# Kernel tuning notes

Measured on AMD Instinct MI355X. Metric: run time of the kernel, lower is better.

Reference implementation:

```python
import jax, jax.numpy as jnp
import numpy as np

N = 38332          # poi_len - 1 nodes
POI_LEN = 38333
GF = 64            # graph_features
POI_DIM = 128
C = 128            # gcn_channel
L = 4              # gcn_layers
OUT = 128          # graph_out_dim
E = N * 16         # edges (avg degree 16)
IN_DIM = POI_DIM * GF // 2 + GF // 2  # 4128


def leaky(x, s):
    return jnp.where(x >= 0, x, s * x)


def _gcn(x, W, b, src, dst):
    # PyG GCNConv: lin -> symmetric deg^{-1/2} norm over self-loop graph -> scatter-sum + bias
    h = x @ W
    deg = jax.ops.segment_sum(jnp.ones(src.shape[0], h.dtype), dst, num_segments=N)
    dinv = jnp.where(deg > 0, jax.lax.rsqrt(deg), 0.0)
    norm = dinv[src] * dinv[dst]
    return jax.ops.segment_sum(h[src] * norm[:, None], dst, num_segments=N) + b


def _gat(x, W, a_src, a_dst, b, src, dst):
    # PyG GATConv (heads=1): per-edge LeakyReLU(0.2) logits, softmax over incoming edges
    h = x @ W
    als = h @ a_src            # [N]
    ald = h @ a_dst            # [N]
    e = leaky(als[src] + ald[dst], 0.2)   # [E+N]
    m = jax.ops.segment_max(e, dst, num_segments=N)
    ex = jnp.exp(e - m[dst])
    s = jax.ops.segment_sum(ex, dst, num_segments=N)
    alpha = ex / s[dst]
    return jax.ops.segment_sum(h[src] * alpha[:, None], dst, num_segments=N) + b


def _gnorm(x, w, b, ms, eps=1e-5):
    # PyG GraphNorm over the single graph (node axis)
    mean = x.mean(axis=0)
    out = x - ms * mean
    var = (out * out).mean(axis=0)
    return w * out * jax.lax.rsqrt(var + eps) + b


def setup_inputs() -> dict:
    key = jax.random.key(0)
    ks = jax.random.split(key, 20)
    d = {}
    d["poi"] = jax.random.randint(ks[0], (N, GF // 2), 0, POI_LEN, dtype=jnp.int32)
    d["distance"] = jax.random.uniform(ks[1], (N, GF // 2), dtype=jnp.float32)
    d["edge_index"] = jax.random.randint(ks[2], (2, E), 0, N, dtype=jnp.int32)
    d["emb_table"] = jax.random.normal(ks[3], (POI_LEN, POI_DIM), dtype=jnp.float32) * 0.05
    d["W_in"] = jax.random.normal(ks[4], (IN_DIM, C), dtype=jnp.float32) * 0.02
    d["b_in"] = jnp.zeros((C,), jnp.float32)
    d["gcn_W"] = jax.random.normal(ks[5], (L, C, C), dtype=jnp.float32) * 0.05
    d["gcn_b"] = jnp.zeros((L, C), jnp.float32)
    d["norm_w"] = jnp.ones((L, C), jnp.float32)
    d["norm_b"] = jnp.zeros((L, C), jnp.float32)
    d["norm_ms"] = jnp.ones((L, C), jnp.float32)
    d["gat_W"] = jax.random.normal(ks[6], (L, C, C), dtype=jnp.float32) * 0.05
    d["gat_asrc"] = jax.random.normal(ks[7], (L, C), dtype=jnp.float32) * 0.05
    d["gat_adst"] = jax.random.normal(ks[8], (L, C), dtype=jnp.float32) * 0.05
    d["gat_b"] = jnp.zeros((L, C), jnp.float32)
    d["W_out"] = jax.random.normal(ks[9], (C, 1), dtype=jnp.float32) * 0.05
    d["b_out"] = jnp.zeros((1,), jnp.float32)
    d["fc1_W"] = jax.random.normal(ks[10], (N, 128), dtype=jnp.float32) * 0.01
    d["fc1_b"] = jnp.zeros((128,), jnp.float32)
    d["fc2_W"] = jax.random.normal(ks[11], (128, OUT), dtype=jnp.float32) * 0.05
    d["fc2_b"] = jnp.zeros((OUT,), jnp.float32)
    return d


def reference(poi, distance, edge_index, emb_table, W_in, b_in, gcn_W, gcn_b,
              norm_w, norm_b, norm_ms, gat_W, gat_asrc, gat_adst, gat_b,
              W_out, b_out, fc1_W, fc1_b, fc2_W, fc2_b):
    loops = jnp.arange(N, dtype=edge_index.dtype)
    src = jnp.concatenate([edge_index[0], loops])   # self loops (PyG default)
    dst = jnp.concatenate([edge_index[1], loops])
    # feature assembly: emb(poi) flattened || distance
    x = jnp.concatenate([emb_table[poi].reshape(N, -1), distance], axis=1)  # [N, 4128]
    x = leaky(_gcn(x, W_in, b_in, src, dst), 0.01)
    for i in range(L):  # GcnUnit: GCN->norm->lrelu->res, GAT->norm->lrelu->res (shared norm params)
        t = _gnorm(_gcn(x, gcn_W[i], gcn_b[i], src, dst), norm_w[i], norm_b[i], norm_ms[i])
        x = x + leaky(t, 0.01)
        t = _gnorm(_gat(x, gat_W[i], gat_asrc[i], gat_adst[i], gat_b[i], src, dst),
                   norm_w[i], norm_b[i], norm_ms[i])
        x = x + leaky(t, 0.01)
    x = leaky(_gcn(x, W_out, b_out, src, dst), 0.01).reshape(-1)  # [N]
    h = leaky(x @ fc1_W + fc1_b, 0.01)
    return h @ fc2_W + fc2_b  # [128]
```

## Files before the change

### kernel.cpp

```cpp
#include <hip/hip_runtime.h>


typedef _Float16 f16;
typedef f16 f16x8 __attribute__((ext_vector_type(8)));
typedef f16 f16x4 __attribute__((ext_vector_type(4)));
typedef f16 f16x2 __attribute__((ext_vector_type(2)));
typedef float f32x4 __attribute__((ext_vector_type(4)));

__device__ __forceinline__ float lrelu(float x, float s){ return x>=0.f? x : s*x; }

__global__ __launch_bounds__(256) void k_deg(const int* __restrict__ dst,
                                             int* __restrict__ deg, int E) {
  int i = blockIdx.x * 256 + threadIdx.x;
  if (i < E) atomicAdd(&deg[dst[i]], 1);
}

__global__ __launch_bounds__(1024) void k_scan1(const int* __restrict__ deg,
    int* __restrict__ row_ptr, int* __restrict__ bsum, float* __restrict__ dinv, int n) {
  int b = blockIdx.x, t = threadIdx.x, i = b * 1024 + t;
  __shared__ int sd[1024];
  int v = (i < n) ? deg[i] : 0;
  if (i < n) dinv[i] = rsqrtf((float)(v + 1));
  sd[t] = v;
  __syncthreads();
  for (int off = 1; off < 1024; off <<= 1) {
    int o = (t >= off) ? sd[t - off] : 0;
    __syncthreads();
    sd[t] += o;
    __syncthreads();
  }
  if (i < n) row_ptr[i + 1] = sd[t];
  if (t == 1023) bsum[b] = sd[1023];
  if (b == 0 && t == 0) row_ptr[0] = 0;
}

__global__ __launch_bounds__(64) void k_scan2(int* __restrict__ bsum, int nb) {
  int lane = threadIdx.x;
  int v = (lane < nb) ? bsum[lane] : 0;
  int x = v;
  for (int off = 1; off < 64; off <<= 1) {
    int o = __shfl_up(x, off, 64);
    if (lane >= off) x += o;
  }
  if (lane < nb) bsum[lane] = x - v;
}

__global__ __launch_bounds__(256) void k_scan3(int* __restrict__ row_ptr,
                                               const int* __restrict__ bsum, int n) {
  int i = blockIdx.x * 256 + threadIdx.x;
  if (i < n) row_ptr[i + 1] += bsum[i >> 10];
}

__global__ __launch_bounds__(256) void k_fill(const int* __restrict__ src,
                                              const int* __restrict__ dst,
                                              const int* __restrict__ row_ptr,
                                              const float* __restrict__ dinv,
                                              int* __restrict__ fill,
                                              int* __restrict__ csr,
                                              float* __restrict__ csrw, int E) {
  int i = blockIdx.x * 256 + threadIdx.x;
  if (i < E) {
    int d = dst[i], s = src[i];
    int pos = row_ptr[d] + atomicAdd(&fill[d], 1);
    csr[pos] = s;
    csrw[pos] = dinv[d] * dinv[s];
  }
}

__global__ __launch_bounds__(256) void k_conv_emb(const float* __restrict__ src,
                                                  f16* __restrict__ dst, int total4) {
  int i = blockIdx.x * 256 + threadIdx.x;
  if (i >= total4) return;
  float4 v = ((const float4*)src)[i];
  f16x4 o = { (f16)v.x, (f16)v.y, (f16)v.z, (f16)v.w };
  ((f16x4*)dst)[i] = o;
}

__global__ __launch_bounds__(256) void k_pack_w(const float* __restrict__ W,
    f16* __restrict__ hi, int kb_total) {
  int idx = blockIdx.x * 256 + threadIdx.x;
  int c = idx & 127, kb = idx >> 7;
  if (kb >= kb_total) return;
  f16x8 hv;
#pragma unroll
  for (int j = 0; j < 8; j++) hv[j] = (f16)W[(size_t)(kb*8 + j) * 128 + c];
  ((f16x8*)hi)[idx] = hv;
}

__global__ __launch_bounds__(256) void k_pack_w8(const float* __restrict__ gcnW,
    const float* __restrict__ gatW, f16* __restrict__ hi, f16* __restrict__ lo) {
  int mat = blockIdx.y;
  const float* W = (mat < 4) ? gcnW + (size_t)mat * 16384 : gatW + (size_t)(mat - 4) * 16384;
  int idx = blockIdx.x * 256 + threadIdx.x;
  int c = idx & 127, kb = idx >> 7;
  f16x8 hv, lv;
#pragma unroll
  for (int j = 0; j < 8; j++) {
    float v = W[(size_t)(kb*8 + j) * 128 + c];
    f16 h = (f16)v;
    hv[j] = h; lv[j] = (f16)(v - (float)h);
  }
  ((f16x8*)hi)[mat * 2048 + idx] = hv;
  ((f16x8*)lo)[mat * 2048 + idx] = lv;
}

#define APAD 152
__global__ __launch_bounds__(512) void k_mfma_embed(const int* __restrict__ poi,
    const float* __restrict__ dist, const f16* __restrict__ eh,
    const f16* __restrict__ wh, f16* __restrict__ H16, int n) {
  __shared__ __attribute__((aligned(16))) char smem[49152];
  int* poi_s = (int*)smem;
  f16* aS    = (f16*)(smem + 8192);
  f16* OT    = (f16*)smem;
  float* F   = (float*)(smem + 16384);
  int tid = threadIdx.x;
  int bn = blockIdx.x * 64;
  int half = tid >> 8;
  int t2 = tid & 255;
  int ln = t2 >> 2, qt = t2 & 3;
  int xrow = bn + ln; if (xrow > n - 1) xrow = n - 1;
  {
#pragma unroll
    for (int jj = 0; jj < 4; jj++)
      poi_s[half * 1024 + (qt * 4 + jj) * 64 + ln] =
        poi[(size_t)xrow * 32 + half * 16 + qt * 4 + jj];
  }
  int w2 = (tid >> 6) & 3, lane = tid & 63;
  int q = lane >> 4, l15 = lane & 15;
  int mtb = (w2 & 1) * 2;
  int ntb = (w2 >> 1) * 4;
  f16* aH = aS + half * 64 * APAD;
  f32x4 acc[2][4];
#pragma unroll
  for (int a = 0; a < 2; a++)
#pragma unroll
    for (int b = 0; b < 4; b++) { acc[a][b][0]=0.f; acc[a][b][1]=0.f; acc[a][b][2]=0.f; acc[a][b][3]=0.f; }
  __syncthreads();

  f16x8 A0, A1, A2, A3, B0, B1, B2, B3;
  {
    const f16* sp = eh + (size_t)poi_s[half * 1024 + 0 * 64 + ln] * 128 + qt * 32;
    A0 = *(const f16x8*)(sp);      A1 = *(const f16x8*)(sp + 8);
    A2 = *(const f16x8*)(sp + 16); A3 = *(const f16x8*)(sp + 24);
  }
  {
    const f16* sp = eh + (size_t)poi_s[half * 1024 + 1 * 64 + ln] * 128 + qt * 32;
    B0 = *(const f16x8*)(sp);      B1 = *(const f16x8*)(sp + 8);
    B2 = *(const f16x8*)(sp + 16); B3 = *(const f16x8*)(sp + 24);
  }
  f16* wp = aH + ln * APAD + qt * 32;

#pragma unroll 1
  for (int jj = 0; jj < 8; jj++) {
    int j0 = jj * 2;
    __syncthreads();
    *(f16x8*)(wp) = A0; *(f16x8*)(wp + 8) = A1;
    *(f16x8*)(wp + 16) = A2; *(f16x8*)(wp + 24) = A3;
    if (jj < 7) {
      const f16* sp = eh + (size_t)poi_s[half * 1024 + (j0 + 2) * 64 + ln] * 128 + qt * 32;
      A0 = *(const f16x8*)(sp);      A1 = *(const f16x8*)(sp + 8);
      A2 = *(const f16x8*)(sp + 16); A3 = *(const f16x8*)(sp + 24);
    }
    __syncthreads();
#pragma unroll
    for (int kcl = 0; kcl < 4; kcl++) {
      f16x8 a_h[2];
#pragma unroll
      for (int mi = 0; mi < 2; mi++)
        a_h[mi] = *(const f16x8*)(aH + ((mtb + mi) * 16 + l15) * APAD + kcl * 32 + q * 8);
      int kb = (half * 16 + j0) * 16 + kcl * 4 + q;
#pragma unroll
      for (int ni = 0; ni < 4; ni++) {
        f16x8 bh = *(const f16x8*)(wh + ((size_t)kb * 128 + (ntb + ni) * 16 + l15) * 8);
#pragma unroll
        for (int mi = 0; mi < 2; mi++)
          acc[mi][ni] = __builtin_amdgcn_mfma_f32_16x16x32_f16(a_h[mi], bh, acc[mi][ni], 0, 0, 0);
      }
    }
    __syncthreads();
    *(f16x8*)(wp) = B0; *(f16x8*)(wp + 8) = B1;
    *(f16x8*)(wp + 16) = B2; *(f16x8*)(wp + 24) = B3;
    if (jj < 7) {
      const f16* sp = eh + (size_t)poi_s[half * 1024 + (j0 + 3) * 64 + ln] * 128 + qt * 32;
      B0 = *(const f16x8*)(sp);      B1 = *(const f16x8*)(sp + 8);
      B2 = *(const f16x8*)(sp + 16); B3 = *(const f16x8*)(sp + 24);
    }
    __syncthreads();
#pragma unroll
    for (int kcl = 0; kcl < 4; kcl++) {
      f16x8 a_h[2];
#pragma unroll
      for (int mi = 0; mi < 2; mi++)
        a_h[mi] = *(const f16x8*)(aH + ((mtb + mi) * 16 + l15) * APAD + kcl * 32 + q * 8);
      int kb = (half * 16 + j0 + 1) * 16 + kcl * 4 + q;
#pragma unroll
      for (int ni = 0; ni < 4; ni++) {
        f16x8 bh = *(const f16x8*)(wh + ((size_t)kb * 128 + (ntb + ni) * 16 + l15) * 8);
#pragma unroll
        for (int mi = 0; mi < 2; mi++)
          acc[mi][ni] = __builtin_amdgcn_mfma_f32_16x16x32_f16(a_h[mi], bh, acc[mi][ni], 0, 0, 0);
      }
    }
  }
  if (half) {
    int nc0 = bn + (mtb + 0) * 16 + l15; if (nc0 > n - 1) nc0 = n - 1;
    int nc1 = bn + (mtb + 1) * 16 + l15; if (nc1 > n - 1) nc1 = n - 1;
    f16x8 ad[2];
#pragma unroll
    for (int mi = 0; mi < 2; mi++) {
      int nc = mi ? nc1 : nc0;
      const float* dp = dist + (size_t)nc * 32 + q * 8;
      float4 d0 = *(const float4*)dp, d1 = *(const float4*)(dp + 4);
      ad[mi][0]=(f16)d0.x; ad[mi][1]=(f16)d0.y; ad[mi][2]=(f16)d0.z; ad[mi][3]=(f16)d0.w;
      ad[mi][4]=(f16)d1.x; ad[mi][5]=(f16)d1.y; ad[mi][6]=(f16)d1.z; ad[mi][7]=(f16)d1.w;
    }
    int kb = 512 + q;
#pragma unroll
    for (int ni = 0; ni < 4; ni++) {
      f16x8 bh = *(const f16x8*)(wh + ((size_t)kb * 128 + (ntb + ni) * 16 + l15) * 8);
#pragma unroll
      for (int mi = 0; mi < 2; mi++)
        acc[mi][ni] = __builtin_amdgcn_mfma_f32_16x16x32_f16(ad[mi], bh, acc[mi][ni], 0, 0, 0);
    }
  }
  __syncthreads();
  if (half) {
#pragma unroll
    for (int mi = 0; mi < 2; mi++)
#pragma unroll
      for (int ni = 0; ni < 4; ni++)
#pragma unroll
        for (int r = 0; r < 4; r++)
          F[((mtb + mi) * 16 + q * 4 + r) * 128 + (ntb + ni) * 16 + l15] = acc[mi][ni][r];
  }
  __syncthreads();
  if (!half) {
#pragma unroll
    for (int mi = 0; mi < 2; mi++)
#pragma unroll
      for (int ni = 0; ni < 4; ni++)
#pragma unroll
        for (int r = 0; r < 4; r++) {
          int o = ((mtb + mi) * 16 + q * 4 + r) * 128 + (ntb + ni) * 16 + l15;
          OT[o] = (f16)(acc[mi][ni][r] + F[o]);
        }
  }
  __syncthreads();
#pragma unroll
  for (int ch = 0; ch < 2; ch++) {
    int c1024 = tid + ch * 512;
    int row = c1024 >> 4, c8 = c1024 & 15;
    if (bn + row < n)
      *(f16x8*)(H16 + (size_t)(bn + row) * 128 + c8 * 8) = *(const f16x8*)(OT + row * 128 + c8 * 8);
  }
}

#define LPAD 136
__global__ __launch_bounds__(256) void k_mfma_lin(const f16* __restrict__ XH,
    const f16* __restrict__ wh, const f16* __restrict__ wl,
    f16* __restrict__ H16, int n,
    const float* __restrict__ asrc, const float* __restrict__ adst,
    float* __restrict__ als, float* __restrict__ ald,
    const float* __restrict__ yres, const float* __restrict__ scA,
    const float* __restrict__ shA, float* __restrict__ xf) {
  __shared__ __attribute__((aligned(16))) char smem[64 * LPAD * 2];
  f16* aS = (f16*)smem;
  f16* ot = (f16*)smem;
  float* dsrc = (float*)(smem + 16384);
  float* ddst = (float*)(smem + 16896);
  int tid = threadIdx.x;
  int bn = blockIdx.x * 64;
  int ln = tid >> 2, qt = tid & 3;
  int w = tid >> 6, lane = tid & 63;
  int q = lane >> 4, l15 = lane & 15;
  int mtb = (w & 1) * 2;
  int ntb = (w >> 1) * 4;
  f16* wp = aS + ln * LPAD + qt * 32;
  if (yres) {
    int row = bn + ln;
    if (row < n) {
      const float4* yp = (const float4*)(yres + (size_t)row * 128 + qt * 32);
      float4* xp = (float4*)(xf + (size_t)row * 128 + qt * 32);
      const float4* scp = (const float4*)(scA + qt * 32);
      const float4* shp = (const float4*)(shA + qt * 32);
#pragma unroll
      for (int jj = 0; jj < 8; jj++) {
        float4 yv = yp[jj], xv = xp[jj], sc = scp[jj], sh = shp[jj];
        xv.x += lrelu(sc.x * yv.x + sh.x, 0.01f);
        xv.y += lrelu(sc.y * yv.y + sh.y, 0.01f);
        xv.z += lrelu(sc.z * yv.z + sh.z, 0.01f);
        xv.w += lrelu(sc.w * yv.w + sh.w, 0.01f);
        xp[jj] = xv;
        f16x4 o = { (f16)xv.x, (f16)xv.y, (f16)xv.z, (f16)xv.w };
        *(f16x4*)(wp + jj * 4) = o;
      }
    } else {
      f16x8 z = {};
#pragma unroll
      for (int jj = 0; jj < 4; jj++) *(f16x8*)(wp + jj * 8) = z;
    }
  } else {
    int xrow = bn + ln; if (xrow > n - 1) xrow = n - 1;
    const f16* srcp = XH + (size_t)xrow * 128 + qt * 32;
    *(f16x8*)(wp)      = *(const f16x8*)(srcp);
    *(f16x8*)(wp + 8)  = *(const f16x8*)(srcp + 8);
    *(f16x8*)(wp + 16) = *(const f16x8*)(srcp + 16);
    *(f16x8*)(wp + 24) = *(const f16x8*)(srcp + 24);
  }
  float av[4], bv[4];
  if (asrc) {
#pragma unroll
    for (int ni = 0; ni < 4; ni++) {
      av[ni] = asrc[(ntb + ni) * 16 + l15];
      bv[ni] = adst[(ntb + ni) * 16 + l15];
    }
  }
  f32x4 acc[2][4];
#pragma unroll
  for (int a = 0; a < 2; a++)
#pragma unroll
    for (int b = 0; b < 4; b++) { acc[a][b][0]=0.f; acc[a][b][1]=0.f; acc[a][b][2]=0.f; acc[a][b][3]=0.f; }
  __syncthreads();
#pragma unroll
  for (int kcl = 0; kcl < 4; kcl++) {
    f16x8 a_h[2];
#pragma unroll
    for (int mi = 0; mi < 2; mi++)
      a_h[mi] = *(const f16x8*)(aS + ((mtb + mi) * 16 + l15) * LPAD + kcl * 32 + q * 8);
    int kb = kcl * 4 + q;
#pragma unroll
    for (int ni = 0; ni < 4; ni++) {
      size_t boff = ((size_t)kb * 128 + (ntb + ni) * 16 + l15) * 8;
      f16x8 bh = *(const f16x8*)(wh + boff);
      f16x8 bl = *(const f16x8*)(wl + boff);
#pragma unroll
      for (int mi = 0; mi < 2; mi++) {
        acc[mi][ni] = __builtin_amdgcn_mfma_f32_16x16x32_f16(a_h[mi], bh, acc[mi][ni], 0, 0, 0);
        acc[mi][ni] = __builtin_amdgcn_mfma_f32_16x16x32_f16(a_h[mi], bl, acc[mi][ni], 0, 0, 0);
      }
    }
  }
  __syncthreads();
  if (asrc) {
#pragma unroll
    for (int mi = 0; mi < 2; mi++)
#pragma unroll
      for (int r = 0; r < 4; r++) {
        float ps = 0.f, pd = 0.f;
#pragma unroll
        for (int ni = 0; ni < 4; ni++) { ps += acc[mi][ni][r] * av[ni]; pd += acc[mi][ni][r] * bv[ni]; }
#pragma unroll
        for (int msk = 8; msk > 0; msk >>= 1) {
          ps += __shfl_xor(ps, msk, 64);
          pd += __shfl_xor(pd, msk, 64);
        }
        if (l15 == 0) {
          int row = (mtb + mi) * 16 + q * 4 + r;
          dsrc[row * 2 + (w >> 1)] = ps;
          ddst[row * 2 + (w >> 1)] = pd;
        }
      }
  }
#pragma unroll
  for (int mi = 0; mi < 2; mi++)
#pragma unroll
    for (int ni = 0; ni < 4; ni++)
#pragma unroll
      for (int r = 0; r < 4; r++)
        ot[((mtb + mi) * 16 + q * 4 + r) * 128 + (ntb + ni) * 16 + l15] = (f16)acc[mi][ni][r];
  __syncthreads();
  if (bn + ln < n) {
    f16* dst = H16 + (size_t)(bn + ln) * 128 + qt * 32;
    const f16* srcp = ot + ln * 128 + qt * 32;
#pragma unroll
    for (int jj = 0; jj < 4; jj++)
      *(f16x8*)(dst + jj * 8) = *(const f16x8*)(srcp + jj * 8);
  }
  if (asrc && tid < 64 && bn + tid < n) {
    als[bn + tid] = dsrc[tid * 2] + dsrc[tid * 2 + 1];
    ald[bn + tid] = ddst[tid * 2] + ddst[tid * 2 + 1];
  }
}

__global__ __launch_bounds__(256) void k_gcn_agg16(const f16x2* __restrict__ H2,
    const float* __restrict__ dinv, const int* __restrict__ row_ptr,
    const int* __restrict__ csr, const float* __restrict__ csrw,
    const float* __restrict__ bias,
    float2* __restrict__ out2, f16x2* __restrict__ xh_out, int n, int leaky_flag,
    float* __restrict__ psum, float* __restrict__ psumsq) {
  int w = threadIdx.x >> 6;
  int node = blockIdx.x * 4 + w;
  int lane = threadIdx.x & 63;
  __shared__ float s1[4][128], s2[4][128];
  float vx = 0.f, vy = 0.f;
  if (node < n) {
    int rs = row_ptr[node], re = row_ptr[node + 1];
    int d = re - rs;
    float dn = dinv[node];
    int  sidx = (lane < d) ? csr[rs + lane]  : 0;
    float swt = (lane < d) ? csrw[rs + lane] : 0.f;
    f16x2 sv = H2[(size_t)node * 64 + lane];
    float ax = dn * dn * (float)sv[0], ay = dn * dn * (float)sv[1];
    int dl = d < 64 ? d : 64;
    int dl8 = (dl + 7) & ~7;
    for (int j = 0; j < dl8; j += 8) {
      int ii[8]; float ww[8];
#pragma unroll
      for (int u = 0; u < 8; u++) {
        ii[u] = __shfl(sidx, j + u, 64);
        ww[u] = __shfl(swt,  j + u, 64);
      }
      f16x2 vv[8];
#pragma unroll
      for (int u = 0; u < 8; u++) vv[u] = H2[(size_t)ii[u] * 64 + lane];
#pragma unroll
      for (int u = 0; u < 8; u++) {
        ax += ww[u] * (float)vv[u][0];
        ay += ww[u] * (float)vv[u][1];
      }
    }
    for (int e = rs + 64; e < re; e++) {
      int s = csr[e]; float wv = csrw[e];
      f16x2 v = H2[(size_t)s * 64 + lane];
      ax += wv * (float)v[0]; ay += wv * (float)v[1];
    }
    float2 bvv = ((const float2*)bias)[lane];
    vx = ax + bvv.x; vy = ay + bvv.y;
    if (leaky_flag) { vx = lrelu(vx, 0.01f); vy = lrelu(vy, 0.01f); }
    out2[(size_t)node * 64 + lane] = make_float2(vx, vy);
    if (xh_out) { f16x2 o = { (f16)vx, (f16)vy }; xh_out[(size_t)node * 64 + lane] = o; }
  }
  if (psum) {
    s1[w][2*lane] = vx;  s1[w][2*lane+1] = vy;
    s2[w][2*lane] = vx*vx; s2[w][2*lane+1] = vy*vy;
    __syncthreads();
    int t = threadIdx.x;
    if (t < 128) {
      float S = s1[0][t] + s1[1][t] + s1[2][t] + s1[3][t];
      float Q = s2[0][t] + s2[1][t] + s2[2][t] + s2[3][t];
      int slot = blockIdx.x & 127;
      atomicAdd(&psum[slot * 128 + t], S);
      atomicAdd(&psumsq[slot * 128 + t], Q);
    }
  }
}

__global__ __launch_bounds__(256) void k_gat_agg16(const f16x2* __restrict__ H2,
    const float* __restrict__ als, const float* __restrict__ ald,
    const int* __restrict__ row_ptr, const int* __restrict__ csr,
    const float* __restrict__ bias, float2* __restrict__ y2, int n,
    float* __restrict__ psum, float* __restrict__ psumsq) {
  int w = threadIdx.x >> 6;
  int node = blockIdx.x * 4 + w;
  int lane = threadIdx.x & 63;
  __shared__ float s1[4][128], s2[4][128];
  float vx = 0.f, vy = 0.f;
  if (node < n) {
    int rs = row_ptr[node], re = row_ptr[node + 1];
    int d = re - rs;
    float aldn = ald[node];
    float e_self = lrelu(als[node] + aldn, 0.2f);
    f16x2 sv = H2[(size_t)node * 64 + lane];
    float ax, ay, sm;
    if (d <= 64) {
      int sidx = (lane < d) ? csr[rs + lane] : 0;
      float e_k = (lane < d) ? lrelu(als[sidx] + aldn, 0.2f) : -3.4e38f;
      float tmx = e_k;
      for (int off = 1; off < 64; off <<= 1) tmx = fmaxf(tmx, __shfl_xor(tmx, off, 64));
      float mx = fmaxf(e_self, tmx);
      float g_k = (lane < d) ? __expf(e_k - mx) : 0.f;
      float tsm = g_k;
      for (int off = 1; off < 64; off <<= 1) tsm += __shfl_xor(tsm, off, 64);
      float ws = __expf(e_self - mx);
      sm = tsm + ws;
      ax = ws * (float)sv[0]; ay = ws * (float)sv[1];
      int d8 = (d + 7) & ~7;
      for (int j = 0; j < d8; j += 8) {
        int ii[8]; float gg[8];
#pragma unroll
        for (int u = 0; u < 8; u++) {
          ii[u] = __shfl(sidx, j + u, 64);
          gg[u] = __shfl(g_k,  j + u, 64);
        }
        f16x2 vv[8];
#pragma unroll
        for (int u = 0; u < 8; u++) vv[u] = H2[(size_t)ii[u] * 64 + lane];
#pragma unroll
        for (int u = 0; u < 8; u++) {
          ax += gg[u] * (float)vv[u][0];
          ay += gg[u] * (float)vv[u][1];
        }
      }
    } else {
      float mx = e_self;
      for (int i = rs + lane; i < re; i += 64) mx = fmaxf(mx, lrelu(als[csr[i]] + aldn, 0.2f));
      for (int off = 1; off < 64; off <<= 1) mx = fmaxf(mx, __shfl_xor(mx, off, 64));
      float ws = __expf(e_self - mx);
      sm = ws;
      ax = ws * (float)sv[0]; ay = ws * (float)sv[1];
      for (int i = rs; i < re; i++) {
        int s = csr[i];
        float g = __expf(lrelu(als[s] + aldn, 0.2f) - mx);
        f16x2 v = H2[(size_t)s * 64 + lane];
        sm += g; ax += g*(float)v[0]; ay += g*(float)v[1];
      }
    }
    float inv_s = 1.f / sm;
    float2 bvv = ((const float2*)bias)[lane];
    vx = ax * inv_s + bvv.x; vy = ay * inv_s + bvv.y;
    y2[(size_t)node * 64 + lane] = make_float2(vx, vy);
  }
  s1[w][2*lane] = vx;  s1[w][2*lane+1] = vy;
  s2[w][2*lane] = vx*vx; s2[w][2*lane+1] = vy*vy;
  __syncthreads();
  int t = threadIdx.x;
  if (t < 128) {
    float S = s1[0][t] + s1[1][t] + s1[2][t] + s1[3][t];
    float Q = s2[0][t] + s2[1][t] + s2[2][t] + s2[3][t];
    int slot = blockIdx.x & 127;
    atomicAdd(&psum[slot * 128 + t], S);
    atomicAdd(&psumsq[slot * 128 + t], Q);
  }
}

__global__ __launch_bounds__(256) void k_stats(const float* __restrict__ psum,
    const float* __restrict__ psumsq, const float* __restrict__ w,
    const float* __restrict__ bb, const float* __restrict__ ms,
    float* __restrict__ scaleA, float* __restrict__ shiftA, int n) {
  int t = threadIdx.x, c = t & 127, half = t >> 7;
  float S = 0.f, Q = 0.f;
  for (int s = half; s < 128; s += 2) { S += psum[s * 128 + c]; Q += psumsq[s * 128 + c]; }
  __shared__ float sh[256], sq[256];
  sh[t] = S; sq[t] = Q;
  __syncthreads();
  if (half == 0) {
    double Sd = (double)sh[c] + (double)sh[c + 128];
    double Qd = (double)sq[c] + (double)sq[c + 128];
    double invn = 1.0 / (double)n;
    double mean = Sd * invn;
    double mt = (double)ms[c] * mean;
    double var = Qd * invn - 2.0 * mt * mean + mt * mt;
    float rstd = rsqrtf((float)var + 1e-5f);
    float sc = w[c] * rstd;
    scaleA[c] = sc;
    shiftA[c] = bb[c] - sc * (float)mt;
  }
}

__global__ __launch_bounds__(256) void k_dot1_res(const float* __restrict__ y,
    const float* __restrict__ scA, const float* __restrict__ shA,
    const float* __restrict__ x, const float* __restrict__ wv,
    float* __restrict__ o, int n) {
  int node = blockIdx.x * 4 + (threadIdx.x >> 6);
  int lane = threadIdx.x & 63;
  if (node >= n) return;
  float2 yv = ((const float2*)y)[(size_t)node * 64 + lane];
  float2 xv = ((const float2*)x)[(size_t)node * 64 + lane];
  float2 sc = ((const float2*)scA)[lane];
  float2 sh = ((const float2*)shA)[lane];
  float hx = xv.x + lrelu(sc.x * yv.x + sh.x, 0.01f);
  float hy = xv.y + lrelu(sc.y * yv.y + sh.y, 0.01f);
  float2 v1 = ((const float2*)wv)[lane];
  float s1 = hx * v1.x + hy * v1.y;
  for (int off = 32; off > 0; off >>= 1) s1 += __shfl_down(s1, off, 64);
  if (lane == 0) o[node] = s1;
}

__global__ __launch_bounds__(256) void k_scalar_agg(const float* __restrict__ xsv,
    const float* __restrict__ dinv, const int* __restrict__ row_ptr,
    const int* __restrict__ csr, const float* __restrict__ csrw,
    const float* __restrict__ b_out, float* __restrict__ xout, int n) {
  int i = blockIdx.x * 256 + threadIdx.x;
  if (i >= n) return;
  float dn = dinv[i];
  float acc = dn * dn * xsv[i];
  int re = row_ptr[i + 1];
  for (int e = row_ptr[i]; e < re; e++)
    acc += csrw[e] * xsv[csr[e]];
  xout[i] = lrelu(acc + b_out[0], 0.01f);
}

__global__ __launch_bounds__(256) void k_fc1(const float* __restrict__ xout,
    const float* __restrict__ fw, float* __restrict__ pfc, int n, int chunk) {
  int b = blockIdx.x, t = threadIdx.x;
  int c = t & 127, half = t >> 7;
  int s0 = b * chunk;
  int s1 = s0 + chunk; if (s1 > n) s1 = n;
  float s = 0.f;
  for (int i = s0 + half; i < s1; i += 2) s += xout[i] * fw[(size_t)i * 128 + c];
  __shared__ float sh[256];
  sh[t] = s; __syncthreads();
  if (half == 0) pfc[b * 128 + c] = sh[c] + sh[c + 128];
}

__global__ __launch_bounds__(128) void k_final(const float* __restrict__ pfc,
    const float* __restrict__ b1, const float* __restrict__ fw2,
    const float* __restrict__ b2, float* __restrict__ out) {
  int c = threadIdx.x;
  float s = 0.f;
  for (int b = 0; b < 128; b++) s += pfc[b * 128 + c];
  float hv = lrelu(s + b1[c], 0.01f);
  __shared__ float h1[128];
  h1[c] = hv; __syncthreads();
  float o = b2[c];
  for (int j = 0; j < 128; j++) o += h1[j] * fw2[j * 128 + c];
  out[c] = o;
}

extern "C" void kernel_launch(void* const* d_in, const int* in_sizes, int n_in,
                              void* d_out, int out_size, void* d_ws, size_t ws_size,
                              hipStream_t stream) {
  const int* poi      = (const int*)d_in[0];
  const float* dist   = (const float*)d_in[1];
  const int* ei       = (const int*)d_in[2];
  const float* emb    = (const float*)d_in[3];
  const float* W_in   = (const float*)d_in[4];
  const float* b_in   = (const float*)d_in[5];
  const float* gcn_W  = (const float*)d_in[6];
  const float* gcn_b  = (const float*)d_in[7];
  const float* norm_w = (const float*)d_in[8];
  const float* norm_b = (const float*)d_in[9];
  const float* norm_ms= (const float*)d_in[10];
  const float* gat_W  = (const float*)d_in[11];
  const float* gat_as = (const float*)d_in[12];
  const float* gat_ad = (const float*)d_in[13];
  const float* gat_b  = (const float*)d_in[14];
  const float* W_out  = (const float*)d_in[15];
  const float* b_out  = (const float*)d_in[16];
  const float* fc1_W  = (const float*)d_in[17];
  const float* fc1_b  = (const float*)d_in[18];
  const float* fc2_W  = (const float*)d_in[19];
  const float* fc2_b  = (const float*)d_in[20];

  const int N   = in_sizes[0] / 32;
  const int E   = in_sizes[2] / 2;
  const int POI = in_sizes[3] / 128;
  const int* srcp = ei;
  const int* dstp = ei + E;
  float* out = (float*)d_out;

  char* p = (char*)d_ws;
  auto alloc = [&](size_t bytes) { char* r = p; p += (bytes + 255) & ~(size_t)255; return r; };
  float* x   = (float*)alloc((size_t)N * 128 * 4);
  f16* h16   = (f16*)alloc((size_t)N * 128 * 2);
  f16* xh    = (f16*)alloc((size_t)N * 128 * 2);
  size_t Rneed = (size_t)POI * 128 * 2;
  size_t Ry    = (size_t)N * 128 * 4;
  char* R = alloc(Rneed > Ry ? Rneed : Ry);
  f16* ehalf = (f16*)R;
  float* y   = (float*)R;
  const int KBIN = 4128 / 8;
  f16* wih = (f16*)alloc((size_t)KBIN * 128 * 8 * 2);
  f16* wsh = (f16*)alloc((size_t)8 * 16384 * 2);
  f16* wsl = (f16*)alloc((size_t)8 * 16384 * 2);
  float* dinv   = (float*)alloc((size_t)N * 4);
  float* als    = (float*)alloc((size_t)N * 4);
  float* ald    = (float*)alloc((size_t)N * 4);
  float* xsv    = (float*)alloc((size_t)N * 4);
  float* xout   = (float*)alloc((size_t)N * 4);
  float* statsbuf = (float*)alloc((size_t)32 * 16384 * 4);
  float* pfc    = (float*)alloc(128 * 128 * 4);
  float* scaleA = (float*)alloc(128 * 4);
  float* shiftA = (float*)alloc(128 * 4);
  int* deg     = (int*)alloc((size_t)N * 2 * 4);
  int* fill    = deg + N;
  int* row_ptr = (int*)alloc(((size_t)N + 1) * 4);
  int* csr     = (int*)alloc((size_t)E * 4);
  float* csrw  = (float*)alloc((size_t)E * 4);
  int* bsum    = (int*)alloc(64 * 4);

  const int chunk = (N + 127) / 128;
  const int gblocks = (N + 63) / 64;
  const int eblocks = (E + 255) / 256;
  const int n4 = N * 32;
  const int nwb = (N + 3) / 4;
  const int nb1024 = (N + 1023) / 1024;
  (void)n4;

  hipMemsetAsync(deg, 0, sizeof(int) * 2 * (size_t)N, stream);
  hipMemsetAsync(statsbuf, 0, (size_t)32 * 16384 * 4, stream);
  k_deg<<<eblocks, 256, 0, stream>>>(dstp, deg, E);
  k_scan1<<<nb1024, 1024, 0, stream>>>(deg, row_ptr, bsum, dinv, N);
  k_scan2<<<1, 64, 0, stream>>>(bsum, nb1024);
  k_scan3<<<(N + 255) / 256, 256, 0, stream>>>(row_ptr, bsum, N);
  k_fill<<<eblocks, 256, 0, stream>>>(srcp, dstp, row_ptr, dinv, fill, csr, csrw, E);

  int et4 = POI * 128 / 4;
  k_conv_emb<<<(et4 + 255) / 256, 256, 0, stream>>>(emb, ehalf, et4);
  k_pack_w<<<(KBIN * 128 + 255) / 256, 256, 0, stream>>>(W_in, wih, KBIN);
  k_pack_w8<<<dim3(8, 8), 256, 0, stream>>>(gcn_W, gat_W, wsh, wsl);

  k_mfma_embed<<<gblocks, 512, 0, stream>>>(poi, dist, ehalf, wih, h16, N);
  k_gcn_agg16<<<nwb, 256, 0, stream>>>((const f16x2*)h16, dinv, row_ptr, csr, csrw, b_in,
                                       (float2*)x, (f16x2*)xh, N, 1, nullptr, nullptr);

  for (int l = 0; l < 4; l++) {
    const f16* gh = wsh + (size_t)l * 16384;
    const f16* gl = wsl + (size_t)l * 16384;
    const f16* th = wsh + (size_t)(4 + l) * 16384;
    const f16* tl = wsl + (size_t)(4 + l) * 16384;
    float* ps0 = statsbuf + (size_t)(4 * l) * 16384;
    float* pq0 = ps0 + 16384;
    float* ps1 = ps0 + 2 * 16384;
    float* pq1 = ps0 + 3 * 16384;
    if (l == 0)
      k_mfma_lin<<<gblocks, 256, 0, stream>>>(xh, gh, gl, h16, N,
          nullptr, nullptr, nullptr, nullptr, nullptr, nullptr, nullptr, nullptr);
    else
      k_mfma_lin<<<gblocks, 256, 0, stream>>>(nullptr, gh, gl, h16, N,
          nullptr, nullptr, nullptr, nullptr, y, scaleA, shiftA, x);
    k_gcn_agg16<<<nwb, 256, 0, stream>>>((const f16x2*)h16, dinv, row_ptr, csr, csrw,
                                         gcn_b + l * 128, (float2*)y, (f16x2*)nullptr, N, 0,
                                         ps0, pq0);
    k_stats<<<1, 256, 0, stream>>>(ps0, pq0, norm_w + l * 128, norm_b + l * 128,
                                   norm_ms + l * 128, scaleA, shiftA, N);
    k_mfma_lin<<<gblocks, 256, 0, stream>>>(nullptr, th, tl, h16, N,
        gat_as + l * 128, gat_ad + l * 128, als, ald, y, scaleA, shiftA, x);
    k_gat_agg16<<<nwb, 256, 0, stream>>>((const f16x2*)h16, als, ald, row_ptr, csr,
                                         gat_b + l * 128, (float2*)y, N, ps1, pq1);
    k_stats<<<1, 256, 0, stream>>>(ps1, pq1, norm_w + l * 128, norm_b + l * 128,
                                   norm_ms + l * 128, scaleA, shiftA, N);
  }

  k_dot1_res<<<nwb, 256, 0, stream>>>(y, scaleA, shiftA, x, W_out, xsv, N);
  k_scalar_agg<<<(N + 255) / 256, 256, 0, stream>>>(xsv, dinv, row_ptr, csr, csrw, b_out, xout, N);
  k_fc1<<<128, 256, 0, stream>>>(xout, fc1_W, pfc, N, chunk);
  k_final<<<1, 128, 0, stream>>>(pfc, fc1_b, fc2_W, fc2_b, out);
}
```

Before: 1.163 ms.

## Fuse GraphNorm stats into aggregation kernels via last-block counter; simplify embed loop

Removes the separate single-block k_stats launches by having the last block to finish each aggregation kernel, detected with an atomic counter, compute the norm scale and shift. This saves eight small kernel launches and their serialization gaps, at the cost of an atomic fence per block and a serial tail on one block. The embedding GEMM loop is also rewritten from a two-buffer unrolled prefetch to a single-register prefetch over 16 iterations, which shortens the code but reduces how far ahead the gathers are issued.

New measurement: 4.534 ms. +289.9%, slower.

```diff
diff --git a/kernel.cpp b/kernel.cpp
--- a/kernel.cpp
+++ b/kernel.cpp
@@ -137,29 +137,23 @@
     for (int b = 0; b < 4; b++) { acc[a][b][0]=0.f; acc[a][b][1]=0.f; acc[a][b][2]=0.f; acc[a][b][3]=0.f; }
   __syncthreads();
 
-  f16x8 A0, A1, A2, A3, B0, B1, B2, B3;
+  f16x8 r0, r1, r2, r3;
   {
-    const f16* sp = eh + (size_t)poi_s[half * 1024 + 0 * 64 + ln] * 128 + qt * 32;
-    A0 = *(const f16x8*)(sp);      A1 = *(const f16x8*)(sp + 8);
-    A2 = *(const f16x8*)(sp + 16); A3 = *(const f16x8*)(sp + 24);
-  }
-  {
-    const f16* sp = eh + (size_t)poi_s[half * 1024 + 1 * 64 + ln] * 128 + qt * 32;
-    B0 = *(const f16x8*)(sp);      B1 = *(const f16x8*)(sp + 8);
-    B2 = *(const f16x8*)(sp + 16); B3 = *(const f16x8*)(sp + 24);
-  }
-  f16* wp = aH + ln * APAD + qt * 32;
+    const f16* srcp = eh + (size_t)poi_s[half * 1024 + ln] * 128 + qt * 32;
+    r0 = *(const f16x8*)(srcp);      r1 = *(const f16x8*)(srcp + 8);
+    r2 = *(const f16x8*)(srcp + 16); r3 = *(const f16x8*)(srcp + 24);
+  }
 
 #pragma unroll 1
-  for (int jj = 0; jj < 8; jj++) {
-    int j0 = jj * 2;
+  for (int j = 0; j < 16; j++) {
     __syncthreads();
-    *(f16x8*)(wp) = A0; *(f16x8*)(wp + 8) = A1;
-    *(f16x8*)(wp + 16) = A2; *(f16x8*)(wp + 24) = A3;
-    if (jj < 7) {
-      const f16* sp = eh + (size_t)poi_s[half * 1024 + (j0 + 2) * 64 + ln] * 128 + qt * 32;
-      A0 = *(const f16x8*)(sp);      A1 = *(const f16x8*)(sp + 8);
-      A2 = *(const f16x8*)(sp + 16); A3 = *(const f16x8*)(sp + 24);
+    f16* wp = aH + ln * APAD + qt * 32;
+    *(f16x8*)(wp) = r0; *(f16x8*)(wp + 8) = r1;
+    *(f16x8*)(wp + 16) = r2; *(f16x8*)(wp + 24) = r3;
+    if (j + 1 < 16) {
+      const f16* srcp = eh + (size_t)poi_s[half * 1024 + (j + 1) * 64 + ln] * 128 + qt * 32;
+      r0 = *(const f16x8*)(srcp);      r1 = *(const f16x8*)(srcp + 8);
+      r2 = *(const f16x8*)(srcp + 16); r3 = *(const f16x8*)(srcp + 24);
     }
     __syncthreads();
 #pragma unroll
@@ -168,31 +162,7 @@
 #pragma unroll
       for (int mi = 0; mi < 2; mi++)
         a_h[mi] = *(const f16x8*)(aH + ((mtb + mi) * 16 + l15) * APAD + kcl * 32 + q * 8);
-      int kb = (half * 16 + j0) * 16 + kcl * 4 + q;
-#pragma unroll
-      for (int ni = 0; ni < 4; ni++) {
-        f16x8 bh = *(const f16x8*)(wh + ((size_t)kb * 128 + (ntb + ni) * 16 + l15) * 8);
-#pragma unroll
-        for (int mi = 0; mi < 2; mi++)
-          acc[mi][ni] = __builtin_amdgcn_mfma_f32_16x16x32_f16(a_h[mi], bh, acc[mi][ni], 0, 0, 0);
-      }
-    }
-    __syncthreads();
-    *(f16x8*)(wp) = B0; *(f16x8*)(wp + 8) = B1;
-    *(f16x8*)(wp + 16) = B2; *(f16x8*)(wp + 24) = B3;
-    if (jj < 7) {
-      const f16* sp = eh + (size_t)poi_s[half * 1024 + (j0 + 3) * 64 + ln] * 128 + qt * 32;
-      B0 = *(const f16x8*)(sp);      B1 = *(const f16x8*)(sp + 8);
-      B2 = *(const f16x8*)(sp + 16); B3 = *(const f16x8*)(sp + 24);
-    }
-    __syncthreads();
-#pragma unroll
-    for (int kcl = 0; kcl < 4; kcl++) {
-      f16x8 a_h[2];
-#pragma unroll
-      for (int mi = 0; mi < 2; mi++)
-        a_h[mi] = *(const f16x8*)(aH + ((mtb + mi) * 16 + l15) * APAD + kcl * 32 + q * 8);
-      int kb = (half * 16 + j0 + 1) * 16 + kcl * 4 + q;
+      int kb = (half * 16 + j) * 16 + kcl * 4 + q;
 #pragma unroll
       for (int ni = 0; ni < 4; ni++) {
         f16x8 bh = *(const f16x8*)(wh + ((size_t)kb * 128 + (ntb + ni) * 16 + l15) * 8);
@@ -382,12 +352,42 @@
   }
 }
 
+__device__ __forceinline__ void stats_tail(const float* __restrict__ psum,
+    const float* __restrict__ psumsq, const float* __restrict__ nw,
+    const float* __restrict__ nbb, const float* __restrict__ nms,
+    float* __restrict__ scaleA, float* __restrict__ shiftA, int n,
+    float* sh2, float* sq2) {
+  int t = threadIdx.x, c = t & 127, half = t >> 7;
+  float S = 0.f, Q = 0.f;
+  for (int s = half; s < 128; s += 2) {
+    S += __hip_atomic_load(&psum[s * 128 + c], __ATOMIC_RELAXED, __HIP_MEMORY_SCOPE_AGENT);
+    Q += __hip_atomic_load(&psumsq[s * 128 + c], __ATOMIC_RELAXED, __HIP_MEMORY_SCOPE_AGENT);
+  }
+  sh2[t] = S; sq2[t] = Q;
+  __syncthreads();
+  if (half == 0) {
+    double Sd = (double)sh2[c] + (double)sh2[c + 128];
+    double Qd = (double)sq2[c] + (double)sq2[c + 128];
+    double invn = 1.0 / (double)n;
+    double mean = Sd * invn;
+    double mt = (double)nms[c] * mean;
+    double var = Qd * invn - 2.0 * mt * mean + mt * mt;
+    float rstd = rsqrtf((float)var + 1e-5f);
+    float sc = nw[c] * rstd;
+    scaleA[c] = sc;
+    shiftA[c] = nbb[c] - sc * (float)mt;
+  }
+}
+
 __global__ __launch_bounds__(256) void k_gcn_agg16(const f16x2* __restrict__ H2,
     const float* __restrict__ dinv, const int* __restrict__ row_ptr,
     const int* __restrict__ csr, const float* __restrict__ csrw,
     const float* __restrict__ bias,
     float2* __restrict__ out2, f16x2* __restrict__ xh_out, int n, int leaky_flag,
-    float* __restrict__ psum, float* __restrict__ psumsq) {
+    float* __restrict__ psum, float* __restrict__ psumsq,
+    const float* __restrict__ nw, const float* __restrict__ nbb,
+    const float* __restrict__ nms, float* __restrict__ scaleA,
+    float* __restrict__ shiftA, int* __restrict__ ctr) {
   int w = threadIdx.x >> 6;
   int node = blockIdx.x * 4 + w;
   int lane = threadIdx.x & 63;
@@ -442,6 +442,16 @@
       atomicAdd(&psum[slot * 128 + t], S);
       atomicAdd(&psumsq[slot * 128 + t], Q);
     }
+    __shared__ int lastFlag;
+    __syncthreads();
+    if (t == 0) {
+      __threadfence();
+      int prev = __hip_atomic_fetch_add(ctr, 1, __ATOMIC_ACQ_REL, __HIP_MEMORY_SCOPE_AGENT);
+      lastFlag = (prev == (int)gridDim.x - 1);
+    }
+    __syncthreads();
+    if (lastFlag)
+      stats_tail(psum, psumsq, nw, nbb, nms, scaleA, shiftA, n, (float*)s1, (float*)s2);
   }
 }
 
@@ -449,7 +459,10 @@
     const float* __restrict__ als, const float* __restrict__ ald,
     const int* __restrict__ row_ptr, const int* __restrict__ csr,
     const float* __restrict__ bias, float2* __restrict__ y2, int n,
-    float* __restrict__ psum, float* __restrict__ psumsq) {
+    float* __restrict__ psum, float* __restrict__ psumsq,
+    const float* __restrict__ nw, const float* __restrict__ nbb,
+    const float* __restrict__ nms, float* __restrict__ scaleA,
+    float* __restrict__ shiftA, int* __restrict__ ctr) {
   int w = threadIdx.x >> 6;
   int node = blockIdx.x * 4 + w;
   int lane = threadIdx.x & 63;
@@ -521,30 +534,16 @@
     atomicAdd(&psum[slot * 128 + t], S);
     atomicAdd(&psumsq[slot * 128 + t], Q);
   }
-}
-
-__global__ __launch_bounds__(256) void k_stats(const float* __restrict__ psum,
-    const float* __restrict__ psumsq, const float* __restrict__ w,
-    const float* __restrict__ bb, const float* __restrict__ ms,
-    float* __restrict__ scaleA, float* __restrict__ shiftA, int n) {
-  int t = threadIdx.x, c = t & 127, half = t >> 7;
-  float S = 0.f, Q = 0.f;
-  for (int s = half; s < 128; s += 2) { S += psum[s * 128 + c]; Q += psumsq[s * 128 + c]; }
-  __shared__ float sh[256], sq[256];
-  sh[t] = S; sq[t] = Q;
-  __syncthreads();
-  if (half == 0) {
-    double Sd = (double)sh[c] + (double)sh[c + 128];
-    double Qd = (double)sq[c] + (double)sq[c + 128];
-    double invn = 1.0 / (double)n;
-    double mean = Sd * invn;
-    double mt = (double)ms[c] * mean;
-    double var = Qd * invn - 2.0 * mt * mean + mt * mt;
-    float rstd = rsqrtf((float)var + 1e-5f);
-    float sc = w[c] * rstd;
-    scaleA[c] = sc;
-    shiftA[c] = bb[c] - sc * (float)mt;
-  }
+  __shared__ int lastFlag;
+  __syncthreads();
+  if (t == 0) {
+    __threadfence();
+    int prev = __hip_atomic_fetch_add(ctr, 1, __ATOMIC_ACQ_REL, __HIP_MEMORY_SCOPE_AGENT);
+    lastFlag = (prev == (int)gridDim.x - 1);
+  }
+  __syncthreads();
+  if (lastFlag)
+    stats_tail(psum, psumsq, nw, nbb, nms, scaleA, shiftA, n, (float*)s1, (float*)s2);
 }
 
 __global__ __launch_bounds__(256) void k_dot1_res(const float* __restrict__ y,
@@ -668,14 +667,13 @@
   int* csr     = (int*)alloc((size_t)E * 4);
   float* csrw  = (float*)alloc((size_t)E * 4);
   int* bsum    = (int*)alloc(64 * 4);
+  int* ctrs    = (int*)(statsbuf + (size_t)16 * 16384);
 
   const int chunk = (N + 127) / 128;
   const int gblocks = (N + 63) / 64;
   const int eblocks = (E + 255) / 256;
-  const int n4 = N * 32;
   const int nwb = (N + 3) / 4;
   const int nb1024 = (N + 1023) / 1024;
-  (void)n4;
 
   hipMemsetAsync(deg, 0, sizeof(int) * 2 * (size_t)N, stream);
   hipMemsetAsync(statsbuf, 0, (size_t)32 * 16384 * 4, stream);
@@ -692,7 +690,8 @@
 
   k_mfma_embed<<<gblocks, 512, 0, stream>>>(poi, dist, ehalf, wih, h16, N);
   k_gcn_agg16<<<nwb, 256, 0, stream>>>((const f16x2*)h16, dinv, row_ptr, csr, csrw, b_in,
-                                       (float2*)x, (f16x2*)xh, N, 1, nullptr, nullptr);
+                                       (float2*)x, (f16x2*)xh, N, 1, nullptr, nullptr,
+                                       nullptr, nullptr, nullptr, nullptr, nullptr, nullptr);
 
   for (int l = 0; l < 4; l++) {
     const f16* gh = wsh + (size_t)l * 16384;
@@ -711,15 +710,14 @@
           nullptr, nullptr, nullptr, nullptr, y, scaleA, shiftA, x);
     k_gcn_agg16<<<nwb, 256, 0, stream>>>((const f16x2*)h16, dinv, row_ptr, csr, csrw,
                                          gcn_b + l * 128, (float2*)y, (f16x2*)nullptr, N, 0,
-                                         ps0, pq0);
-    k_stats<<<1, 256, 0, stream>>>(ps0, pq0, norm_w + l * 128, norm_b + l * 128,
-                                   norm_ms + l * 128, scaleA, shiftA, N);
+                                         ps0, pq0, norm_w + l * 128, norm_b + l * 128,
+                                         norm_ms + l * 128, scaleA, shiftA, ctrs + 2 * l);
     k_mfma_lin<<<gblocks, 256, 0, stream>>>(nullptr, th, tl, h16, N,
         gat_as + l * 128, gat_ad + l * 128, als, ald, y, scaleA, shiftA, x);
     k_gat_agg16<<<nwb, 256, 0, stream>>>((const f16x2*)h16, als, ald, row_ptr, csr,
-                                         gat_b + l * 128, (float2*)y, N, ps1, pq1);
-    k_stats<<<1, 256, 0, stream>>>(ps1, pq1, norm_w + l * 128, norm_b + l * 128,
-                                   norm_ms + l * 128, scaleA, shiftA, N);
+                                         gat_b + l * 128, (float2*)y, N, ps1, pq1,
+                                         norm_w + l * 128, norm_b + l * 128,
+                                         norm_ms + l * 128, scaleA, shiftA, ctrs + 2 * l + 1);
   }
 
   k_dot1_res<<<nwb, 256, 0, stream>>>(y, scaleA, shiftA, x, W_out, xsv, N);
```

## Fuse GraphNorm stats reduction into linear kernels and simplify embed prefetch loop

Applied to the files above, without the earlier changes.

Removes the single-block k_stats launches between aggregation and the next linear layer. Each k_mfma_lin block now reduces the partial sums itself and computes the scale/shift in shared memory, using double precision for the variance. This cuts 7 serialized tiny launches but makes every block redo the 128x128 partial-sum reduction. The embed GEMM also drops its two-register-set A/B double prefetch in favour of a single-buffer 16-iteration loop, which lowers register use but shortens the prefetch distance.

Measured after the change: 981.2 us. -15.6%, faster.

```diff
diff --git a/kernel.cpp b/kernel.cpp
--- a/kernel.cpp
+++ b/kernel.cpp
@@ -137,29 +137,23 @@
     for (int b = 0; b < 4; b++) { acc[a][b][0]=0.f; acc[a][b][1]=0.f; acc[a][b][2]=0.f; acc[a][b][3]=0.f; }
   __syncthreads();
 
-  f16x8 A0, A1, A2, A3, B0, B1, B2, B3;
+  f16x8 r0, r1, r2, r3;
   {
-    const f16* sp = eh + (size_t)poi_s[half * 1024 + 0 * 64 + ln] * 128 + qt * 32;
-    A0 = *(const f16x8*)(sp);      A1 = *(const f16x8*)(sp + 8);
-    A2 = *(const f16x8*)(sp + 16); A3 = *(const f16x8*)(sp + 24);
-  }
-  {
-    const f16* sp = eh + (size_t)poi_s[half * 1024 + 1 * 64 + ln] * 128 + qt * 32;
-    B0 = *(const f16x8*)(sp);      B1 = *(const f16x8*)(sp + 8);
-    B2 = *(const f16x8*)(sp + 16); B3 = *(const f16x8*)(sp + 24);
-  }
-  f16* wp = aH + ln * APAD + qt * 32;
+    const f16* srcp = eh + (size_t)poi_s[half * 1024 + ln] * 128 + qt * 32;
+    r0 = *(const f16x8*)(srcp);      r1 = *(const f16x8*)(srcp + 8);
+    r2 = *(const f16x8*)(srcp + 16); r3 = *(const f16x8*)(srcp + 24);
+  }
 
 #pragma unroll 1
-  for (int jj = 0; jj < 8; jj++) {
-    int j0 = jj * 2;
+  for (int j = 0; j < 16; j++) {
     __syncthreads();
-    *(f16x8*)(wp) = A0; *(f16x8*)(wp + 8) = A1;
-    *(f16x8*)(wp + 16) = A2; *(f16x8*)(wp + 24) = A3;
-    if (jj < 7) {
-      const f16* sp = eh + (size_t)poi_s[half * 1024 + (j0 + 2) * 64 + ln] * 128 + qt * 32;
-      A0 = *(const f16x8*)(sp);      A1 = *(const f16x8*)(sp + 8);
-      A2 = *(const f16x8*)(sp + 16); A3 = *(const f16x8*)(sp + 24);
+    f16* wp = aH + ln * APAD + qt * 32;
+    *(f16x8*)(wp) = r0; *(f16x8*)(wp + 8) = r1;
+    *(f16x8*)(wp + 16) = r2; *(f16x8*)(wp + 24) = r3;
+    if (j + 1 < 16) {
+      const f16* srcp = eh + (size_t)poi_s[half * 1024 + (j + 1) * 64 + ln] * 128 + qt * 32;
+      r0 = *(const f16x8*)(srcp);      r1 = *(const f16x8*)(srcp + 8);
+      r2 = *(const f16x8*)(srcp + 16); r3 = *(const f16x8*)(srcp + 24);
     }
     __syncthreads();
 #pragma unroll
@@ -168,31 +162,7 @@
 #pragma unroll
       for (int mi = 0; mi < 2; mi++)
         a_h[mi] = *(const f16x8*)(aH + ((mtb + mi) * 16 + l15) * APAD + kcl * 32 + q * 8);
-      int kb = (half * 16 + j0) * 16 + kcl * 4 + q;
-#pragma unroll
-      for (int ni = 0; ni < 4; ni++) {
-        f16x8 bh = *(const f16x8*)(wh + ((size_t)kb * 128 + (ntb + ni) * 16 + l15) * 8);
-#pragma unroll
-        for (int mi = 0; mi < 2; mi++)
-          acc[mi][ni] = __builtin_amdgcn_mfma_f32_16x16x32_f16(a_h[mi], bh, acc[mi][ni], 0, 0, 0);
-      }
-    }
-    __syncthreads();
-    *(f16x8*)(wp) = B0; *(f16x8*)(wp + 8) = B1;
-    *(f16x8*)(wp + 16) = B2; *(f16x8*)(wp + 24) = B3;
-    if (jj < 7) {
-      const f16* sp = eh + (size_t)poi_s[half * 1024 + (j0 + 3) * 64 + ln] * 128 + qt * 32;
-      B0 = *(const f16x8*)(sp);      B1 = *(const f16x8*)(sp + 8);
-      B2 = *(const f16x8*)(sp + 16); B3 = *(const f16x8*)(sp + 24);
-    }
-    __syncthreads();
-#pragma unroll
-    for (int kcl = 0; kcl < 4; kcl++) {
-      f16x8 a_h[2];
-#pragma unroll
-      for (int mi = 0; mi < 2; mi++)
-        a_h[mi] = *(const f16x8*)(aH + ((mtb + mi) * 16 + l15) * APAD + kcl * 32 + q * 8);
-      int kb = (half * 16 + j0 + 1) * 16 + kcl * 4 + q;
+      int kb = (half * 16 + j) * 16 + kcl * 4 + q;
 #pragma unroll
       for (int ni = 0; ni < 4; ni++) {
         f16x8 bh = *(const f16x8*)(wh + ((size_t)kb * 128 + (ntb + ni) * 16 + l15) * 8);
@@ -261,13 +231,19 @@
     f16* __restrict__ H16, int n,
     const float* __restrict__ asrc, const float* __restrict__ adst,
     float* __restrict__ als, float* __restrict__ ald,
-    const float* __restrict__ yres, const float* __restrict__ scA,
-    const float* __restrict__ shA, float* __restrict__ xf) {
-  __shared__ __attribute__((aligned(16))) char smem[64 * LPAD * 2];
+    const float* __restrict__ yres, const float* __restrict__ ps,
+    const float* __restrict__ pq, const float* __restrict__ nw,
+    const float* __restrict__ nbb, const float* __restrict__ nms,
+    float* __restrict__ xf) {
+  __shared__ __attribute__((aligned(16))) char smem[64 * LPAD * 2 + 3072];
   f16* aS = (f16*)smem;
   f16* ot = (f16*)smem;
   float* dsrc = (float*)(smem + 16384);
   float* ddst = (float*)(smem + 16896);
+  float* scf  = (float*)(smem + 17408);
+  float* shf  = scf + 128;
+  float* sst1 = (float*)(smem + 18432);
+  float* sst2 = sst1 + 256;
   int tid = threadIdx.x;
   int bn = blockIdx.x * 64;
   int ln = tid >> 2, qt = tid & 3;
@@ -277,12 +253,32 @@
   int ntb = (w >> 1) * 4;
   f16* wp = aS + ln * LPAD + qt * 32;
   if (yres) {
+    {
+      int c = tid & 127, hf = tid >> 7;
+      float S = 0.f, Q = 0.f;
+      for (int s = hf; s < 128; s += 2) { S += ps[s * 128 + c]; Q += pq[s * 128 + c]; }
+      sst1[tid] = S; sst2[tid] = Q;
+      __syncthreads();
+      if (hf == 0) {
+        double Sd = (double)sst1[c] + (double)sst1[c + 128];
+        double Qd = (double)sst2[c] + (double)sst2[c + 128];
+        double invn = 1.0 / (double)n;
+        double mean = Sd * invn;
+        double mt = (double)nms[c] * mean;
+        double var = Qd * invn - 2.0 * mt * mean + mt * mt;
+        float rstd = rsqrtf((float)var + 1e-5f);
+        float sc = nw[c] * rstd;
+        scf[c] = sc;
+        shf[c] = nbb[c] - sc * (float)mt;
+      }
+      __syncthreads();
+    }
     int row = bn + ln;
     if (row < n) {
       const float4* yp = (const float4*)(yres + (size_t)row * 128 + qt * 32);
       float4* xp = (float4*)(xf + (size_t)row * 128 + qt * 32);
-      const float4* scp = (const float4*)(scA + qt * 32);
-      const float4* shp = (const float4*)(shA + qt * 32);
+      const float4* scp = (const float4*)(scf + qt * 32);
+      const float4* shp = (const float4*)(shf + qt * 32);
 #pragma unroll
       for (int jj = 0; jj < 8; jj++) {
         float4 yv = yp[jj], xv = xp[jj], sc = scp[jj], sh = shp[jj];
@@ -346,17 +342,17 @@
     for (int mi = 0; mi < 2; mi++)
 #pragma unroll
       for (int r = 0; r < 4; r++) {
-        float ps = 0.f, pd = 0.f;
-#pragma unroll
-        for (int ni = 0; ni < 4; ni++) { ps += acc[mi][ni][r] * av[ni]; pd += acc[mi][ni][r] * bv[ni]; }
+        float ps2 = 0.f, pd = 0.f;
+#pragma unroll
+        for (int ni = 0; ni < 4; ni++) { ps2 += acc[mi][ni][r] * av[ni]; pd += acc[mi][ni][r] * bv[ni]; }
 #pragma unroll
         for (int msk = 8; msk > 0; msk >>= 1) {
-          ps += __shfl_xor(ps, msk, 64);
+          ps2 += __shfl_xor(ps2, msk, 64);
           pd += __shfl_xor(pd, msk, 64);
         }
         if (l15 == 0) {
           int row = (mtb + mi) * 16 + q * 4 + r;
-          dsrc[row * 2 + (w >> 1)] = ps;
+          dsrc[row * 2 + (w >> 1)] = ps2;
           ddst[row * 2 + (w >> 1)] = pd;
         }
       }
@@ -672,10 +668,8 @@
   const int chunk = (N + 127) / 128;
   const int gblocks = (N + 63) / 64;
   const int eblocks = (E + 255) / 256;
-  const int n4 = N * 32;
   const int nwb = (N + 3) / 4;
   const int nb1024 = (N + 1023) / 1024;
-  (void)n4;
 
   hipMemsetAsync(deg, 0, sizeof(int) * 2 * (size_t)N, stream);
   hipMemsetAsync(statsbuf, 0, (size_t)32 * 16384 * 4, stream);
@@ -705,23 +699,32 @@
     float* pq1 = ps0 + 3 * 16384;
     if (l == 0)
       k_mfma_lin<<<gblocks, 256, 0, stream>>>(xh, gh, gl, h16, N,
-          nullptr, nullptr, nullptr, nullptr, nullptr, nullptr, nullptr, nullptr);
-    else
+          nullptr, nullptr, nullptr, nullptr,
+          nullptr, nullptr, nullptr, nullptr, nullptr, nullptr, nullptr);
+    else {
+      float* ps1p = statsbuf + (size_t)(4 * (l - 1) + 2) * 16384;
+      float* pq1p = ps1p + 16384;
       k_mfma_lin<<<gblocks, 256, 0, stream>>>(nullptr, gh, gl, h16, N,
-          nullptr, nullptr, nullptr, nullptr, y, scaleA, shiftA, x);
+          nullptr, nullptr, nullptr, nullptr,
+          y, ps1p, pq1p, norm_w + (l - 1) * 128, norm_b + (l - 1) * 128,
+          norm_ms + (l - 1) * 128, x);
+    }
     k_gcn_agg16<<<nwb, 256, 0, stream>>>((const f16x2*)h16, dinv, row_ptr, csr, csrw,
                                          gcn_b + l * 128, (float2*)y, (f16x2*)nullptr, N, 0,
                                          ps0, pq0);
-    k_stats<<<1, 256, 0, stream>>>(ps0, pq0, norm_w + l * 128, norm_b + l * 128,
-                                   norm_ms + l * 128, scaleA, shiftA, N);
     k_mfma_lin<<<gblocks, 256, 0, stream>>>(nullptr, th, tl, h16, N,
-        gat_as + l * 128, gat_ad + l * 128, als, ald, y, scaleA, shiftA, x);
+        gat_as + l * 128, gat_ad + l * 128, als, ald,
+        y, ps0, pq0, norm_w + l * 128, norm_b + l * 128, norm_ms + l * 128, x);
     k_gat_agg16<<<nwb, 256, 0, stream>>>((const f16x2*)h16, als, ald, row_ptr, csr,
                                          gat_b + l * 128, (float2*)y, N, ps1, pq1);
-    k_stats<<<1, 256, 0, stream>>>(ps1, pq1, norm_w + l * 128, norm_b + l * 128,
-                                   norm_ms + l * 128, scaleA, shiftA, N);
-  }
-
+  }
+
+  {
+    float* ps1 = statsbuf + (size_t)(4 * 3 + 2) * 16384;
+    float* pq1 = ps1 + 16384;
+    k_stats<<<1, 256, 0, stream>>>(ps1, pq1, norm_w + 3 * 128, norm_b + 3 * 128,
+                                   norm_ms + 3 * 128, scaleA, shiftA, N);
+  }
   k_dot1_res<<<nwb, 256, 0, stream>>>(y, scaleA, shiftA, x, W_out, xsv, N);
   k_scalar_agg<<<(N + 255) / 256, 256, 0, stream>>>(xsv, dinv, row_ptr, csr, csrw, b_out, xout, N);
   k_fc1<<<128, 256, 0, stream>>>(xout, fc1_W, pfc, N, chunk);
```
